# Performance work log

Hardware: AMD Instinct MI355X
Metric: run time of the kernel (lower is better)

## Reference

```python
import jax, jax.numpy as jnp
import numpy as np

B, S, D, H, F, E, TOPK, W = 1, 4096, 768, 12, 3072, 7, 2, 256  # W = one-sided window


def _layer_norm(x, g, b, eps=1e-5):
    m = jnp.mean(x, -1, keepdims=True)
    v = jnp.var(x, -1, keepdims=True)
    return (x - m) * jax.lax.rsqrt(v + eps) * g + b


def _sliding_attn(x, Wq, bq, Wk, bk, Wv, bv):
    # Longformer sliding-window attention, chunked (no dense SxS matrix).
    Bx, Sx, Dx = x.shape
    Dh = Dx // H
    def proj(Wm, bm):
        return (x @ Wm + bm).reshape(Bx, Sx, H, Dh).transpose(0, 2, 1, 3)  # [B,H,S,Dh]
    q = proj(Wq, bq) * (1.0 / np.sqrt(Dh))
    k = proj(Wk, bk)
    v = proj(Wv, bv)
    nc = Sx // W
    kp = jnp.pad(k, ((0, 0), (0, 0), (W, W), (0, 0)))
    vp = jnp.pad(v, ((0, 0), (0, 0), (W, W), (0, 0)))
    # each query chunk of W tokens sees a 3W key window
    idx = (jnp.arange(nc) * W)[:, None] + jnp.arange(3 * W)[None, :]  # [nc,3W]
    kc = kp[:, :, idx]  # [B,H,nc,3W,Dh]
    vc = vp[:, :, idx]
    qc = q.reshape(Bx, H, nc, W, Dh)
    scores = jnp.einsum('bhcqd,bhckd->bhcqk', qc, kc)  # [B,H,nc,W,3W]
    qi = jnp.arange(W)[:, None]
    ki = jnp.arange(3 * W)[None, :]
    band = (ki >= qi) & (ki <= qi + 2 * W)  # |key_pos - query_pos| <= W
    pos = (jnp.arange(nc) * W)[:, None, None] + ki[None] - W  # global key pos
    valid = band[None] & (pos >= 0) & (pos < Sx)  # [nc,W,3W]
    scores = jnp.where(valid[None, None], scores, -1e9)
    probs = jax.nn.softmax(scores, axis=-1)
    out = jnp.einsum('bhcqk,bhckd->bhcqd', probs, vc)
    return out.reshape(Bx, H, Sx, Dh).transpose(0, 2, 1, 3).reshape(Bx, Sx, Dx)


def setup_inputs() -> dict:
    key = jax.random.key(0)
    ks = jax.random.split(key, 16)
    sc = 0.02
    rn = lambda k, shp: jax.random.normal(k, shp, jnp.float32) * sc
    return {
        'hidden_states': jax.random.normal(ks[0], (B, S, D), jnp.float32),
        'Wq': rn(ks[1], (D, D)), 'bq': jnp.zeros((D,), jnp.float32),
        'Wk': rn(ks[2], (D, D)), 'bk': jnp.zeros((D,), jnp.float32),
        'Wv': rn(ks[3], (D, D)), 'bv': jnp.zeros((D,), jnp.float32),
        'Wo': rn(ks[4], (D, D)), 'bo': jnp.zeros((D,), jnp.float32),
        'ln1_g': jnp.ones((D,), jnp.float32), 'ln1_b': jnp.zeros((D,), jnp.float32),
        'gate_W': rn(ks[5], (D, E)), 'gate_b': jnp.zeros((E,), jnp.float32),
        'W1e': rn(ks[6], (E, D, F)), 'b1e': jnp.zeros((E, F), jnp.float32),
        'W2e': rn(ks[7], (E, F, D)), 'b2e': jnp.zeros((E, D), jnp.float32),
        'Wd': rn(ks[8], (D, D)), 'bd': jnp.zeros((D,), jnp.float32),
        'ln2_g': jnp.ones((D,), jnp.float32), 'ln2_b': jnp.zeros((D,), jnp.float32),
    }


def reference(hidden_states, Wq, bq, Wk, bk, Wv, bv, Wo, bo, ln1_g, ln1_b,
              gate_W, gate_b, W1e, b1e, W2e, b2e, Wd, bd, ln2_g, ln2_b):
    # attention + SelfOutput (dense + residual + LN); dropout = identity (eval)
    attn = _sliding_attn(hidden_states, Wq, bq, Wk, bk, Wv, bv)
    attention_output = _layer_norm(attn @ Wo + bo + hidden_states, ln1_g, ln1_b)
    # MoE feed-forward: dense all-experts compute, top-k masked softmax gate
    gate_logits = attention_output @ gate_W + gate_b  # [B,S,E]
    topv, topi = jax.lax.top_k(gate_logits, TOPK)
    # softmax over (-inf scatter of topk) == softmax over topk values scattered back
    sw = jax.nn.softmax(topv, axis=-1)  # [B,S,k]
    gate_weights = jnp.einsum('bske,bsk->bse',
                              jax.nn.one_hot(topi, E, dtype=attention_output.dtype), sw)
    h = jax.nn.gelu(jnp.einsum('bsd,edf->bsef', attention_output, W1e) + b1e,
                    approximate=False)  # [B,S,E,F]
    eo = jnp.einsum('bsef,efd->bsed', h, W2e) + b2e  # [B,S,E,D]
    moe = jnp.einsum('bsed,bse->bsd', eo, gate_weights)
    ffn = moe @ Wd + bd
    layer_output = _layer_norm(ffn + attention_output, ln2_g, ln2_b)
    return layer_output, gate_weights
```

## Files before the change

### kernel.cpp

```cpp
#include <hip/hip_runtime.h>
#include <math.h>

#define S_LEN 4096
#define DMODEL 768
#define NHEADS 12
#define DH 64
#define FDIM 3072
#define NEXP 7
#define NPAIR (2*S_LEN)
#define MAXTILES 40

typedef _Float16 f16x8 __attribute__((ext_vector_type(8)));
typedef float f32x4 __attribute__((ext_vector_type(4)));

__device__ __forceinline__ unsigned short f2h(float f){
  union { _Float16 h; unsigned short u; } v; v.h = (_Float16)f; return v.u;
}
__device__ __forceinline__ float gelu_f(float x){
  return 0.5f * x * (1.0f + erff(x * 0.7071067811865475f));
}
__device__ __forceinline__ f32x4 mfma16(f16x8 a, f16x8 b, f32x4 c){
  return __builtin_amdgcn_mfma_f32_16x16x32_f16(a, b, c, 0, 0, 0);
}
__device__ __forceinline__ void glds16(const void* g, void* l){
  __builtin_amdgcn_global_load_lds((const __attribute__((address_space(1))) unsigned*)g,
                                   (__attribute__((address_space(3))) unsigned*)l, 16, 0, 0);
}
__device__ __forceinline__ int xcd_logical(int lin, int total){
  int q = total >> 3;
  return (lin & 7)*q + (lin >> 3);
}

__global__ __launch_bounds__(256) void split_kernel(const float* __restrict__ in,
    unsigned short* __restrict__ out, int n){
  int i = blockIdx.x*256 + threadIdx.x;
  if (i >= n) return;
  out[i] = f2h(in[i]);
}

__global__ __launch_bounds__(256) void transp_kernel(const float* __restrict__ in,
    unsigned short* __restrict__ out,
    int R, int C, long inStride, long outStride){
  const float* ip = in + (long)blockIdx.z * inStride;
  long ob = (long)blockIdx.z * outStride;
  __shared__ float tile[32][33];
  int c0 = blockIdx.x*32, r0 = blockIdx.y*32;
  int tx = threadIdx.x, ty = threadIdx.y;
  for (int i = ty; i < 32; i += 8)
    tile[i][tx] = ip[(long)(r0+i)*C + c0 + tx];
  __syncthreads();
  int t  = tx + ty*32;
  int sx = t & 15;
  int sc = t >> 4;
  #pragma unroll
  for (int j = 0; j < 2; j++){
    int cc = sc + j*16;
    float v0 = tile[sx*2][cc], v1 = tile[sx*2+1][cc];
    long oidx = ob + (long)(c0+cc)*R + r0 + sx*2;
    unsigned uh = (unsigned)f2h(v0) | ((unsigned)f2h(v1) << 16);
    *(unsigned*)(out + oidx) = uh;
  }
}

struct GemmP {
  const unsigned short* A;
  const unsigned short* B;
  int M, N, K;
  const float* bias;  const float* bias2; const float* bias3;
  const float* resid;
  float* outF;
  unsigned short* outBF;
  unsigned short *qh,*kh,*vth;
  const int* pair_token;
  const float* pair_w;
  const int* cnt;
  const int* offs;
  const int* tile_e;
  const int* tile_m;
  const int* ntiles;
};

template<int MODE>
__global__ __launch_bounds__(256, 2) void gemm_bt(GemmP p){
  const int tid  = threadIdx.x;
  const int lane = tid & 63;
  const int wave = tid >> 6;
  const int quad = lane >> 4;
  const int ln   = lane & 15;
  const int wr = wave >> 1, wc = wave & 1;
  const int lin = blockIdx.y * gridDim.x + blockIdx.x;
  const int logical = xcd_logical(lin, gridDim.x*gridDim.y);
  const int bn0 = (logical % gridDim.x) * 128;
  const int bm0 = (logical / gridDim.x) * 128;
  const int K = p.K;

  long aoff[2]; long boff[2]; int koff[2];
  #pragma unroll
  for (int j = 0; j < 2; j++){
    int c = tid + j*256;
    int row = c >> 2;
    koff[j] = (c & 3) * 8;
    aoff[j] = (long)(bm0 + row) * K;
    boff[j] = (long)(bn0 + row) * K;
  }

  __shared__ __align__(16) unsigned short As[2][128*32];
  __shared__ __align__(16) unsigned short Bs[2][128*32];

  auto stage = [&](int k0, int buf){
    #pragma unroll
    for (int j = 0; j < 2; j++){
      int c = tid + j*256;
      glds16(p.A + aoff[j] + k0 + koff[j], &As[buf][c*8]);
      glds16(p.B + boff[j] + k0 + koff[j], &Bs[buf][c*8]);
    }
  };

  f32x4 zero4 = {0.f, 0.f, 0.f, 0.f};
  f32x4 acc[4][4];
  #pragma unroll
  for (int i = 0; i < 4; i++)
    #pragma unroll
    for (int j = 0; j < 4; j++) acc[i][j] = zero4;

  stage(0, 0);
  __syncthreads();
  int cur = 0;

  for (int k0 = 0; k0 < K; k0 += 32){
    if (k0 + 32 < K) stage(k0 + 32, cur ^ 1);
    f16x8 af[4], bfr[4];
    #pragma unroll
    for (int mt = 0; mt < 4; mt++)
      af[mt] = *(const f16x8*)&As[cur][(wr*64 + mt*16 + ln)*32 + quad*8];
    #pragma unroll
    for (int nt = 0; nt < 4; nt++)
      bfr[nt] = *(const f16x8*)&Bs[cur][(wc*64 + nt*16 + ln)*32 + quad*8];
    __builtin_amdgcn_s_setprio(1);
    #pragma unroll
    for (int mt = 0; mt < 4; mt++)
      #pragma unroll
      for (int nt = 0; nt < 4; nt++)
        acc[mt][nt] = mfma16(af[mt], bfr[nt], acc[mt][nt]);
    __builtin_amdgcn_s_setprio(0);
    asm volatile("s_waitcnt vmcnt(0)" ::: "memory");
    __builtin_amdgcn_s_barrier();
    cur ^= 1;
  }

  #pragma unroll
  for (int mt = 0; mt < 4; mt++){
    #pragma unroll
    for (int nt = 0; nt < 4; nt++){
      #pragma unroll
      for (int r = 0; r < 4; r++){
        int gm = bm0 + wr*64 + mt*16 + quad*4 + r;
        int gn = bn0 + wc*64 + nt*16 + ln;
        float v = acc[mt][nt][r];
        if (MODE == 0){
          int which = gn >= 1536 ? 2 : (gn >= 768 ? 1 : 0);
          int nn = gn - which*768;
          int hh = nn >> 6, dh = nn & 63;
          if (which == 0){
            float q = (v + p.bias[nn]) * 0.125f;
            long o = ((long)hh*S_LEN + gm)*64 + dh;
            p.qh[o] = f2h(q);
          } else if (which == 1){
            float kv = v + p.bias2[nn];
            long o = ((long)hh*S_LEN + gm)*64 + dh;
            p.kh[o] = f2h(kv);
          } else {
            float vv = v + p.bias3[nn];
            long o = ((long)hh*64 + dh)*S_LEN + gm;
            p.vth[o] = f2h(vv);
          }
        } else if (MODE == 1 || MODE == 4){
          long i = (long)gm*DMODEL + gn;
          p.outF[i] = v + p.bias[gn] + p.resid[i];
        }
      }
    }
  }
}

template<int MODE>
__global__ __launch_bounds__(512, 4) void gemm_big(GemmP p){
  const int lin = blockIdx.y * gridDim.x + blockIdx.x;
  const int logical = xcd_logical(lin, gridDim.x*gridDim.y);
  const int bx = logical % gridDim.x;
  const int ty = logical / gridDim.x;
  if (ty >= *p.ntiles) return;
  const int e   = p.tile_e[ty];
  const int bm0 = p.tile_m[ty];

  const int tid  = threadIdx.x;
  const int lane = tid & 63;
  const int wave = tid >> 6;
  const int quad = lane >> 4;
  const int ln   = lane & 15;
  const int wr = wave >> 1, wc = wave & 1;
  const int bn0 = bx * 128;
  const int K = p.K;

  const int eoff = p.offs[e];
  const int Mloc = p.cnt[e];
  const unsigned short* Bp = p.B + (long)e * FDIM * DMODEL;

  long aoff[2]; int koffA[2];
  #pragma unroll
  for (int j = 0; j < 2; j++){
    int c = tid + j*512;
    int row = c >> 2;
    koffA[j] = (c & 3) * 8;
    int r = bm0 + row; if (r >= Mloc) r = Mloc - 1;
    aoff[j] = (MODE == 2) ? (long)p.pair_token[eoff + r] * K : (long)(eoff + r) * K;
  }
  long boff; int koffB;
  {
    int row = tid >> 2;
    koffB = (tid & 3) * 8;
    boff = (long)(bn0 + row) * K;
  }

  __shared__ __align__(16) unsigned short As[2][256*32];
  __shared__ __align__(16) unsigned short Bs[2][128*32];

  auto stage = [&](int k0, int buf){
    #pragma unroll
    for (int j = 0; j < 2; j++){
      int c = tid + j*512;
      glds16(p.A + aoff[j] + k0 + koffA[j], &As[buf][c*8]);
    }
    glds16(Bp + boff + k0 + koffB, &Bs[buf][tid*8]);
  };

  f32x4 zero4 = {0.f, 0.f, 0.f, 0.f};
  f32x4 acc[4][4];
  #pragma unroll
  for (int i = 0; i < 4; i++)
    #pragma unroll
    for (int j = 0; j < 4; j++) acc[i][j] = zero4;

  stage(0, 0);
  __syncthreads();
  int cur = 0;

  for (int k0 = 0; k0 < K; k0 += 32){
    if (k0 + 32 < K) stage(k0 + 32, cur ^ 1);
    f16x8 af[4], bfr[4];
    #pragma unroll
    for (int mt = 0; mt < 4; mt++)
      af[mt] = *(const f16x8*)&As[cur][(wr*64 + mt*16 + ln)*32 + quad*8];
    #pragma unroll
    for (int nt = 0; nt < 4; nt++)
      bfr[nt] = *(const f16x8*)&Bs[cur][(wc*64 + nt*16 + ln)*32 + quad*8];
    __builtin_amdgcn_s_setprio(1);
    #pragma unroll
    for (int mt = 0; mt < 4; mt++)
      #pragma unroll
      for (int nt = 0; nt < 4; nt++)
        acc[mt][nt] = mfma16(af[mt], bfr[nt], acc[mt][nt]);
    __builtin_amdgcn_s_setprio(0);
    asm volatile("s_waitcnt vmcnt(0)" ::: "memory");
    __builtin_amdgcn_s_barrier();
    cur ^= 1;
  }

  #pragma unroll
  for (int mt = 0; mt < 4; mt++){
    #pragma unroll
    for (int nt = 0; nt < 4; nt++){
      #pragma unroll
      for (int r = 0; r < 4; r++){
        int gm = bm0 + wr*64 + mt*16 + quad*4 + r;
        int gn = bn0 + wc*64 + nt*16 + ln;
        if (gm < Mloc){
          float v = acc[mt][nt][r];
          if (MODE == 2){
            v = gelu_f(v + p.bias[(long)e*FDIM + gn]);
            p.outBF[(long)(eoff + gm)*FDIM + gn] = f2h(v);
          } else {
            int pi = eoff + gm;
            p.outF[(long)pi*DMODEL + gn] = v + p.bias[(long)e*DMODEL + gn];
          }
        }
      }
    }
  }
}

__global__ __launch_bounds__(256) void attn_mfma(
    const unsigned short* __restrict__ Qh,
    const unsigned short* __restrict__ Kh,
    const unsigned short* __restrict__ Vth,
    unsigned short* __restrict__ attn_h){
  const int c = blockIdx.x, h = blockIdx.y, qb = blockIdx.z;
  const int tid = threadIdx.x;
  const int lane = tid & 63, w = tid >> 6;
  const int quad = lane >> 4, ln = lane & 15;
  const int q0 = c*256 + qb*64;
  const int qw = q0 + w*16;

  __shared__ __align__(16) unsigned short Ks[64*64];
  __shared__ __align__(16) unsigned short Vs[64*64];
  __shared__ __align__(16) unsigned short Ps[4][16*72];

  f16x8 qf[2];
  {
    long qrow = ((long)h*S_LEN + qw + ln)*64 + quad*8;
    qf[0] = *(const f16x8*)(Qh + qrow);
    qf[1] = *(const f16x8*)(Qh + qrow + 32);
  }

  float m_s[4], l_s[4];
  f32x4 Oc[4];
  f32x4 z4 = {0.f,0.f,0.f,0.f};
  #pragma unroll
  for (int r = 0; r < 4; r++){ m_s[r] = -1e30f; l_s[r] = 0.f; }
  #pragma unroll
  for (int nt = 0; nt < 4; nt++) Oc[nt] = z4;

  const unsigned short* KB = Kh + (long)h*S_LEN*64;
  const unsigned short* VB = Vth + (long)h*64*S_LEN;

  for (int kb = 0; kb < 12; kb++){
    const int kstart = c*256 - 256 + kb*64;
    if (kstart + 63 < 0 || kstart >= S_LEN) continue;
    if (kstart + 63 < q0 - 256 || kstart > q0 + 63 + 256) continue;
    __syncthreads();
    #pragma unroll
    for (int p2 = 0; p2 < 2; p2++){
      int idx = p2*256 + tid;
      int row = idx >> 3;
      int pc  = idx & 7;
      int lc  = pc ^ (row & 7);
      int ka = kstart + row;
      int kac = ka < 0 ? 0 : (ka > S_LEN-1 ? S_LEN-1 : ka);
      long gK = (long)kac*64 + lc*8;
      glds16(KB + gK, &Ks[idx*8]);
      int ks0 = kstart + lc*8;
      ks0 = ks0 < 0 ? 0 : (ks0 > S_LEN-8 ? S_LEN-8 : ks0);
      long gV = (long)row*S_LEN + ks0;
      glds16(VB + gV, &Vs[idx*8]);
    }
    __syncthreads();
    if (kstart + 63 < qw - 256 || kstart > qw + 15 + 256) continue;

    f32x4 Sc[4];
    #pragma unroll
    for (int nt = 0; nt < 4; nt++) Sc[nt] = z4;
    #pragma unroll
    for (int kc = 0; kc < 2; kc++){
      f16x8 bh[4];
      #pragma unroll
      for (int nt = 0; nt < 4; nt++){
        int row = nt*16 + ln;
        int o = row*64 + (((kc*4 + quad) ^ (row & 7))*8);
        bh[nt] = *(const f16x8*)&Ks[o];
      }
      #pragma unroll
      for (int nt = 0; nt < 4; nt++)
        Sc[nt] = mfma16(qf[kc], bh[nt], Sc[nt]);
    }
    bool interior = (kstart >= qw - 241) && (kstart <= qw + 193) &&
                    (kstart >= 0) && (kstart + 63 <= S_LEN - 1);
    if (!interior){
      #pragma unroll
      for (int nt = 0; nt < 4; nt++){
        int ka = kstart + nt*16 + ln;
        #pragma unroll
        for (int r = 0; r < 4; r++){
          int qa = qw + quad*4 + r;
          bool v = (ka >= 0) && (ka < S_LEN) && (ka >= qa - 256) && (ka <= qa + 256);
          if (!v) Sc[nt][r] = -3.0e38f;
        }
      }
    }
    float bm[4];
    #pragma unroll
    for (int r = 0; r < 4; r++)
      bm[r] = fmaxf(fmaxf(Sc[0][r], Sc[1][r]), fmaxf(Sc[2][r], Sc[3][r]));
    #pragma unroll
    for (int off = 1; off < 16; off <<= 1)
      #pragma unroll
      for (int r = 0; r < 4; r++) bm[r] = fmaxf(bm[r], __shfl_xor(bm[r], off));
    float al[4];
    #pragma unroll
    for (int r = 0; r < 4; r++){
      float mnew = fmaxf(m_s[r], bm[r]);
      al[r] = __expf(m_s[r] - mnew);
      m_s[r] = mnew;
    }
    float psum[4] = {0.f,0.f,0.f,0.f};
    #pragma unroll
    for (int nt = 0; nt < 4; nt++){
      #pragma unroll
      for (int r = 0; r < 4; r++){
        float pv = __expf(Sc[nt][r] - m_s[r]);
        psum[r] += pv;
        int o = (quad*4 + r)*72 + nt*16 + ln;
        Ps[w][o] = f2h(pv);
      }
    }
    #pragma unroll
    for (int off = 1; off < 16; off <<= 1)
      #pragma unroll
      for (int r = 0; r < 4; r++) psum[r] += __shfl_xor(psum[r], off);
    #pragma unroll
    for (int r = 0; r < 4; r++) l_s[r] = l_s[r]*al[r] + psum[r];
    #pragma unroll
    for (int nt = 0; nt < 4; nt++)
      #pragma unroll
      for (int r = 0; r < 4; r++) Oc[nt][r] *= al[r];
    asm volatile("s_waitcnt lgkmcnt(0)" ::: "memory");
    #pragma unroll
    for (int kc = 0; kc < 2; kc++){
      f16x8 ph = *(const f16x8*)&Ps[w][ln*72 + kc*32 + quad*8];
      #pragma unroll
      for (int nt = 0; nt < 4; nt++){
        int row = nt*16 + ln;
        int o = row*64 + (((kc*4 + quad) ^ (row & 7))*8);
        f16x8 vh = *(const f16x8*)&Vs[o];
        Oc[nt] = mfma16(ph, vh, Oc[nt]);
      }
    }
  }
  float inv[4];
  #pragma unroll
  for (int r = 0; r < 4; r++) inv[r] = 1.f / l_s[r];
  #pragma unroll
  for (int nt = 0; nt < 4; nt++){
    #pragma unroll
    for (int r = 0; r < 4; r++){
      int qa = qw + quad*4 + r;
      long o = (long)qa*DMODEL + h*64 + nt*16 + ln;
      attn_h[o] = f2h(Oc[nt][r] * inv[r]);
    }
  }
}

__global__ __launch_bounds__(256) void ln_kernel(const float* __restrict__ x,
    const float* __restrict__ g, const float* __restrict__ b,
    float* __restrict__ outF, unsigned short* __restrict__ outH){
  int s = blockIdx.x;
  const float* row = x + (long)s*DMODEL;
  int t = threadIdx.x;
  float v0 = row[t], v1 = row[t+256], v2 = row[t+512];
  float sum = v0+v1+v2;
  float sq  = v0*v0 + v1*v1 + v2*v2;
  for (int o = 32; o > 0; o >>= 1){ sum += __shfl_xor(sum, o); sq += __shfl_xor(sq, o); }
  __shared__ float s1[4], s2[4];
  int wv = t >> 6;
  if ((t & 63) == 0){ s1[wv] = sum; s2[wv] = sq; }
  __syncthreads();
  sum = s1[0]+s1[1]+s1[2]+s1[3];
  sq  = s2[0]+s2[1]+s2[2]+s2[3];
  float mean = sum * (1.0f/DMODEL);
  float var  = sq  * (1.0f/DMODEL) - mean*mean;
  float inv = rsqrtf(var + 1e-5f);
  float* orow = outF + (long)s*DMODEL;
  unsigned short* hrow = outH ? outH + (long)s*DMODEL : (unsigned short*)0;
  #pragma unroll
  for (int j = 0; j < 3; j++){
    int d = t + j*256;
    float y = (row[d] - mean) * inv * g[d] + b[d];
    orow[d] = y;
    if (hrow) hrow[d] = f2h(y);
  }
}

__global__ __launch_bounds__(256) void gate_kernel(const float* __restrict__ x,
    const float* __restrict__ gw, const float* __restrict__ gb,
    float* __restrict__ gate_out, int* __restrict__ tok_e,
    float* __restrict__ tok_w){
  int w = threadIdx.x >> 6;
  int lane = threadIdx.x & 63;
  int s = blockIdx.x*4 + w;
  float acc[NEXP];
  #pragma unroll
  for (int e = 0; e < NEXP; e++) acc[e] = 0.f;
  const float* xr = x + (long)s*DMODEL;
  #pragma unroll
  for (int j = 0; j < DMODEL/64; j++){
    int d = lane + j*64;
    float xv = xr[d];
    const float* wr = gw + (long)d*NEXP;
    #pragma unroll
    for (int e = 0; e < NEXP; e++) acc[e] += xv * wr[e];
  }
  #pragma unroll
  for (int e = 0; e < NEXP; e++){
    float v = acc[e];
    for (int o = 32; o > 0; o >>= 1) v += __shfl_xor(v, o);
    acc[e] = v;
  }
  if (lane == 0){
    #pragma unroll
    for (int e = 0; e < NEXP; e++) acc[e] += gb[e];
    int i0 = 0;
    for (int e = 1; e < NEXP; e++) if (acc[e] > acc[i0]) i0 = e;
    int i1 = -1;
    for (int e = 0; e < NEXP; e++) if (e != i0 && (i1 < 0 || acc[e] > acc[i1])) i1 = e;
    float e1 = expf(acc[i1] - acc[i0]);
    float inv = 1.f / (1.f + e1);
    float w0 = inv, w1 = e1 * inv;
    float* go = gate_out + (long)s*NEXP;
    #pragma unroll
    for (int e = 0; e < NEXP; e++) go[e] = 0.f;
    go[i0] = w0; go[i1] = w1;
    tok_e[s*2] = i0; tok_e[s*2+1] = i1;
    tok_w[s*2] = w0; tok_w[s*2+1] = w1;
  }
}

__global__ __launch_bounds__(256) void route_kernel(const int* __restrict__ tok_e,
    const float* __restrict__ tok_w,
    int* __restrict__ cnt, int* __restrict__ offs,
    int* __restrict__ pair_token, float* __restrict__ pair_w, int* __restrict__ tok_pi,
    int* __restrict__ tile_e, int* __restrict__ tile_m, int* __restrict__ ntiles){
  __shared__ int hist[256][NEXP];
  __shared__ int cntS[NEXP], offsS[NEXP];
  const int t = threadIdx.x;
  const int CH = NPAIR/256;
  const int base = t*CH;
  #pragma unroll
  for (int e = 0; e < NEXP; e++) hist[t][e] = 0;
  for (int i = 0; i < CH; i++)
    hist[t][tok_e[base+i]]++;
  __syncthreads();
  if (t < NEXP){
    int s = 0;
    for (int i = 0; i < 256; i++){ int v = hist[i][t]; hist[i][t] = s; s += v; }
    cntS[t] = s;
  }
  __syncthreads();
  if (t == 0){
    int s = 0, tt = 0;
    for (int e = 0; e < NEXP; e++){ offsS[e] = s; s += cntS[e]; }
    for (int e = 0; e < NEXP; e++)
      for (int m0 = 0; m0 < cntS[e]; m0 += 256){ tile_e[tt] = e; tile_m[tt] = m0; tt++; }
    *ntiles = tt;
    for (int e = 0; e < NEXP; e++){ cnt[e] = cntS[e]; offs[e] = offsS[e]; }
  }
  __syncthreads();
  for (int i = 0; i < CH; i++){
    int idx = base + i;
    int e = tok_e[idx];
    int pi = offsS[e] + hist[t][e]++;
    pair_token[pi] = idx >> 1;
    pair_w[pi] = tok_w[idx];
    tok_pi[idx] = pi;
  }
}

__global__ __launch_bounds__(256) void combine_kernel(const float* __restrict__ Pbuf,
    const int* __restrict__ tok_pi, const float* __restrict__ tok_w,
    unsigned short* __restrict__ moe_h){
  int t = blockIdx.x;
  int d = threadIdx.x;
  float w0 = tok_w[t*2], w1 = tok_w[t*2+1];
  long p0 = (long)tok_pi[t*2]   * DMODEL;
  long p1 = (long)tok_pi[t*2+1] * DMODEL;
  unsigned short* orow = moe_h + (long)t*DMODEL;
  #pragma unroll
  for (int j = 0; j < 3; j++){
    int dd = d + j*256;
    orow[dd] = f2h(w0*Pbuf[p0+dd] + w1*Pbuf[p1+dd]);
  }
}

extern "C" void kernel_launch(void* const* d_in, const int* in_sizes, int n_in,
                              void* d_out, int out_size, void* d_ws, size_t ws_size,
                              hipStream_t stream){
  (void)in_sizes; (void)n_in; (void)out_size; (void)ws_size;
  const float* hidden = (const float*)d_in[0];
  const float* Wq  = (const float*)d_in[1];
  const float* bq  = (const float*)d_in[2];
  const float* Wk  = (const float*)d_in[3];
  const float* bk  = (const float*)d_in[4];
  const float* Wv  = (const float*)d_in[5];
  const float* bv  = (const float*)d_in[6];
  const float* Wo  = (const float*)d_in[7];
  const float* bo  = (const float*)d_in[8];
  const float* ln1g = (const float*)d_in[9];
  const float* ln1b = (const float*)d_in[10];
  const float* gateW = (const float*)d_in[11];
  const float* gateB = (const float*)d_in[12];
  const float* W1e = (const float*)d_in[13];
  const float* b1e = (const float*)d_in[14];
  const float* W2e = (const float*)d_in[15];
  const float* b2e = (const float*)d_in[16];
  const float* Wd  = (const float*)d_in[17];
  const float* bd  = (const float*)d_in[18];
  const float* ln2g = (const float*)d_in[19];
  const float* ln2b = (const float*)d_in[20];

  float* outL = (float*)d_out;
  float* outG = outL + (size_t)S_LEN*DMODEL;

  const size_t SD = (size_t)S_LEN*DMODEL;
  char* base = (char*)d_ws;
  size_t off = 0;
  auto alloc = [&](size_t bytes)->void*{
    void* r = base + off;
    off = (off + bytes + 255) & ~(size_t)255;
    return r;
  };
  unsigned short* x_h     = (unsigned short*)alloc(SD*2);
  unsigned short* wqkv_h  = (unsigned short*)alloc((size_t)2304*768*2);
  unsigned short* wo_h    = (unsigned short*)alloc((size_t)768*768*2);
  unsigned short* wd_h    = (unsigned short*)alloc((size_t)768*768*2);
  unsigned short* w1_h    = (unsigned short*)alloc((size_t)NEXP*FDIM*DMODEL*2);
  unsigned short* w2_h    = (unsigned short*)alloc((size_t)NEXP*FDIM*DMODEL*2);
  unsigned short* q_h   = (unsigned short*)alloc(SD*2);
  unsigned short* k_h   = (unsigned short*)alloc(SD*2);
  unsigned short* vt_h  = (unsigned short*)alloc(SD*2);
  unsigned short* attn_h = (unsigned short*)alloc(SD*2);
  float* preLN1    = (float*)alloc(SD*4);
  float* attnout_f = (float*)alloc(SD*4);
  unsigned short* attnout_h = (unsigned short*)alloc(SD*2);
  int*   tok_e = (int*)alloc(2*S_LEN*4);
  float* tok_w = (float*)alloc(2*S_LEN*4);
  int*   tok_pi = (int*)alloc(2*S_LEN*4);
  int*   cnt   = (int*)alloc(32*4);
  int*   offs  = (int*)alloc(32*4);
  int*   tile_e = (int*)alloc(MAXTILES*4);
  int*   tile_m = (int*)alloc(MAXTILES*4);
  int*   ntiles = (int*)alloc(4);
  int*   pair_token = (int*)alloc(NPAIR*4);
  float* pair_w     = (float*)alloc(NPAIR*4);
  unsigned short* Hbuf = (unsigned short*)alloc((size_t)NPAIR*FDIM*2);
  float* Pbuf = (float*)alloc((size_t)NPAIR*DMODEL*4);
  unsigned short* moe_h = (unsigned short*)alloc(SD*2);
  float* preLN2 = preLN1;

  split_kernel<<<dim3((unsigned)(SD/256)), dim3(256), 0, stream>>>(hidden, x_h, (int)SD);
  transp_kernel<<<dim3(24,24,1), dim3(32,8), 0, stream>>>(Wq, wqkv_h,           DMODEL, DMODEL, 0, 0);
  transp_kernel<<<dim3(24,24,1), dim3(32,8), 0, stream>>>(Wk, wqkv_h+768*768,   DMODEL, DMODEL, 0, 0);
  transp_kernel<<<dim3(24,24,1), dim3(32,8), 0, stream>>>(Wv, wqkv_h+2*768*768, DMODEL, DMODEL, 0, 0);
  transp_kernel<<<dim3(24,24,1), dim3(32,8), 0, stream>>>(Wo, wo_h, DMODEL, DMODEL, 0, 0);
  transp_kernel<<<dim3(24,24,1), dim3(32,8), 0, stream>>>(Wd, wd_h, DMODEL, DMODEL, 0, 0);
  transp_kernel<<<dim3(96,24,NEXP), dim3(32,8), 0, stream>>>(W1e, w1_h, DMODEL, FDIM, (long)DMODEL*FDIM, (long)DMODEL*FDIM);
  transp_kernel<<<dim3(24,96,NEXP), dim3(32,8), 0, stream>>>(W2e, w2_h, FDIM, DMODEL, (long)DMODEL*FDIM, (long)DMODEL*FDIM);

  GemmP pq = {};
  pq.A = x_h; pq.B = wqkv_h;
  pq.M = S_LEN; pq.N = 2304; pq.K = DMODEL;
  pq.bias = bq; pq.bias2 = bk; pq.bias3 = bv;
  pq.qh = q_h; pq.kh = k_h; pq.vth = vt_h;
  gemm_bt<0><<<dim3(18,32,1), dim3(256), 0, stream>>>(pq);

  attn_mfma<<<dim3(16,NHEADS,4), dim3(256), 0, stream>>>(q_h, k_h, vt_h, attn_h);

  GemmP pw = {};
  pw.A = attn_h; pw.B = wo_h;
  pw.M = S_LEN; pw.N = DMODEL; pw.K = DMODEL;
  pw.bias = bo; pw.resid = hidden; pw.outF = preLN1;
  gemm_bt<1><<<dim3(6,32,1), dim3(256), 0, stream>>>(pw);

  ln_kernel<<<dim3(S_LEN), dim3(256), 0, stream>>>(preLN1, ln1g, ln1b, attnout_f, attnout_h);

  gate_kernel<<<dim3(S_LEN/4), dim3(256), 0, stream>>>(attnout_f, gateW, gateB, outG, tok_e, tok_w);
  route_kernel<<<dim3(1), dim3(256), 0, stream>>>(tok_e, tok_w, cnt, offs,
      pair_token, pair_w, tok_pi, tile_e, tile_m, ntiles);

  GemmP p1 = {};
  p1.A = attnout_h; p1.B = w1_h; p1.M = S_LEN; p1.N = FDIM; p1.K = DMODEL;
  p1.bias = b1e; p1.outBF = Hbuf;
  p1.pair_token = pair_token; p1.cnt = cnt; p1.offs = offs;
  p1.tile_e = tile_e; p1.tile_m = tile_m; p1.ntiles = ntiles;
  gemm_big<2><<<dim3(24,MAXTILES), dim3(512), 0, stream>>>(p1);

  GemmP p2 = {};
  p2.A = Hbuf; p2.B = w2_h; p2.M = S_LEN; p2.N = DMODEL; p2.K = FDIM;
  p2.bias = b2e; p2.outF = Pbuf;
  p2.pair_token = pair_token; p2.pair_w = pair_w; p2.cnt = cnt; p2.offs = offs;
  p2.tile_e = tile_e; p2.tile_m = tile_m; p2.ntiles = ntiles;
  gemm_big<3><<<dim3(6,MAXTILES), dim3(512), 0, stream>>>(p2);

  combine_kernel<<<dim3(S_LEN), dim3(256), 0, stream>>>(Pbuf, tok_pi, tok_w, moe_h);
  GemmP pd = {};
  pd.A = moe_h; pd.B = wd_h; pd.M = S_LEN; pd.N = DMODEL; pd.K = DMODEL;
  pd.bias = bd; pd.resid = attnout_f; pd.outF = preLN2;
  gemm_bt<4><<<dim3(6,32,1), dim3(256), 0, stream>>>(pd);

  ln_kernel<<<dim3(S_LEN), dim3(256), 0, stream>>>(preLN2, ln2g, ln2b, outL, nullptr);
}
```

Before: 601.5 us.

## Swizzle GEMM LDS tiles, batch weight transposes, interleave MoE tile schedule

XOR-swizzles the 16-byte chunk position within each 32-element LDS row in both GEMM kernels, so the MFMA fragment reads spread across LDS banks instead of conflicting. Merges the five 768x768 weight transposes into one launch using a pointer table indexed by blockIdx.z. Reorders the MoE tile list into a strided interleave with -1 sentinels for empty slots, so consecutive blocks work on different experts and empty tiles exit early. The swizzle has to match between the global-to-LDS write and the fragment read, and the scatter into 8 groups of 5 slots assumes there are at most 40 tiles.

```diff
diff --git a/kernel.cpp b/kernel.cpp
--- a/kernel.cpp
+++ b/kernel.cpp
@@ -57,6 +57,29 @@
     int cc = sc + j*16;
     float v0 = tile[sx*2][cc], v1 = tile[sx*2+1][cc];
     long oidx = ob + (long)(c0+cc)*R + r0 + sx*2;
+    unsigned uh = (unsigned)f2h(v0) | ((unsigned)f2h(v1) << 16);
+    *(unsigned*)(out + oidx) = uh;
+  }
+}
+
+struct T5P { const float* in[5]; unsigned short* out[5]; };
+__global__ __launch_bounds__(256) void transp5_kernel(T5P p){
+  const float* ip = p.in[blockIdx.z];
+  unsigned short* out = p.out[blockIdx.z];
+  __shared__ float tile[32][33];
+  int c0 = blockIdx.x*32, r0 = blockIdx.y*32;
+  int tx = threadIdx.x, ty = threadIdx.y;
+  for (int i = ty; i < 32; i += 8)
+    tile[i][tx] = ip[(long)(r0+i)*DMODEL + c0 + tx];
+  __syncthreads();
+  int t  = tx + ty*32;
+  int sx = t & 15;
+  int sc = t >> 4;
+  #pragma unroll
+  for (int j = 0; j < 2; j++){
+    int cc = sc + j*16;
+    float v0 = tile[sx*2][cc], v1 = tile[sx*2+1][cc];
+    long oidx = (long)(c0+cc)*DMODEL + r0 + sx*2;
     unsigned uh = (unsigned)f2h(v0) | ((unsigned)f2h(v1) << 16);
     *(unsigned*)(out + oidx) = uh;
   }
@@ -99,7 +122,8 @@
   for (int j = 0; j < 2; j++){
     int c = tid + j*256;
     int row = c >> 2;
-    koff[j] = (c & 3) * 8;
+    int pc  = c & 3;
+    koff[j] = (pc ^ ((row >> 1) & 3)) * 8;
     aoff[j] = (long)(bm0 + row) * K;
     boff[j] = (long)(bn0 + row) * K;
   }
@@ -127,15 +151,17 @@
   __syncthreads();
   int cur = 0;
 
+  const int rsw = (quad ^ ((ln >> 1) & 3)) * 8;
+
   for (int k0 = 0; k0 < K; k0 += 32){
     if (k0 + 32 < K) stage(k0 + 32, cur ^ 1);
     f16x8 af[4], bfr[4];
     #pragma unroll
     for (int mt = 0; mt < 4; mt++)
-      af[mt] = *(const f16x8*)&As[cur][(wr*64 + mt*16 + ln)*32 + quad*8];
+      af[mt] = *(const f16x8*)&As[cur][(wr*64 + mt*16 + ln)*32 + rsw];
     #pragma unroll
     for (int nt = 0; nt < 4; nt++)
-      bfr[nt] = *(const f16x8*)&Bs[cur][(wc*64 + nt*16 + ln)*32 + quad*8];
+      bfr[nt] = *(const f16x8*)&Bs[cur][(wc*64 + nt*16 + ln)*32 + rsw];
     __builtin_amdgcn_s_setprio(1);
     #pragma unroll
     for (int mt = 0; mt < 4; mt++)
@@ -189,8 +215,8 @@
   const int logical = xcd_logical(lin, gridDim.x*gridDim.y);
   const int bx = logical % gridDim.x;
   const int ty = logical / gridDim.x;
-  if (ty >= *p.ntiles) return;
   const int e   = p.tile_e[ty];
+  if (e < 0) return;
   const int bm0 = p.tile_m[ty];
 
   const int tid  = threadIdx.x;
@@ -211,14 +237,16 @@
   for (int j = 0; j < 2; j++){
     int c = tid + j*512;
     int row = c >> 2;
-    koffA[j] = (c & 3) * 8;
+    int pc  = c & 3;
+    koffA[j] = (pc ^ ((row >> 1) & 3)) * 8;
     int r = bm0 + row; if (r >= Mloc) r = Mloc - 1;
     aoff[j] = (MODE == 2) ? (long)p.pair_token[eoff + r] * K : (long)(eoff + r) * K;
   }
   long boff; int koffB;
   {
     int row = tid >> 2;
-    koffB = (tid & 3) * 8;
+    int pc  = tid & 3;
+    koffB = (pc ^ ((row >> 1) & 3)) * 8;
     boff = (long)(bn0 + row) * K;
   }
 
@@ -245,15 +273,17 @@
   __syncthreads();
   int cur = 0;
 
+  const int rsw = (quad ^ ((ln >> 1) & 3)) * 8;
+
   for (int k0 = 0; k0 < K; k0 += 32){
     if (k0 + 32 < K) stage(k0 + 32, cur ^ 1);
     f16x8 af[4], bfr[4];
     #pragma unroll
     for (int mt = 0; mt < 4; mt++)
-      af[mt] = *(const f16x8*)&As[cur][(wr*64 + mt*16 + ln)*32 + quad*8];
+      af[mt] = *(const f16x8*)&As[cur][(wr*64 + mt*16 + ln)*32 + rsw];
     #pragma unroll
     for (int nt = 0; nt < 4; nt++)
-      bfr[nt] = *(const f16x8*)&Bs[cur][(wc*64 + nt*16 + ln)*32 + quad*8];
+      bfr[nt] = *(const f16x8*)&Bs[cur][(wc*64 + nt*16 + ln)*32 + rsw];
     __builtin_amdgcn_s_setprio(1);
     #pragma unroll
     for (int mt = 0; mt < 4; mt++)
@@ -536,9 +566,15 @@
   __syncthreads();
   if (t == 0){
     int s = 0, tt = 0;
+    int te[MAXTILES], tm[MAXTILES];
     for (int e = 0; e < NEXP; e++){ offsS[e] = s; s += cntS[e]; }
     for (int e = 0; e < NEXP; e++)
-      for (int m0 = 0; m0 < cntS[e]; m0 += 256){ tile_e[tt] = e; tile_m[tt] = m0; tt++; }
+      for (int m0 = 0; m0 < cntS[e]; m0 += 256){ te[tt] = e; tm[tt] = m0; tt++; }
+    for (int p2 = 0; p2 < MAXTILES; p2++){ tile_e[p2] = -1; tile_m[p2] = 0; }
+    for (int t2 = 0; t2 < tt; t2++){
+      int pos = (t2 & 7)*(MAXTILES/8) + (t2 >> 3);
+      tile_e[pos] = te[t2]; tile_m[pos] = tm[t2];
+    }
     *ntiles = tt;
     for (int e = 0; e < NEXP; e++){ cnt[e] = cntS[e]; offs[e] = offsS[e]; }
   }
@@ -635,11 +671,13 @@
   float* preLN2 = preLN1;
 
   split_kernel<<<dim3((unsigned)(SD/256)), dim3(256), 0, stream>>>(hidden, x_h, (int)SD);
-  transp_kernel<<<dim3(24,24,1), dim3(32,8), 0, stream>>>(Wq, wqkv_h,           DMODEL, DMODEL, 0, 0);
-  transp_kernel<<<dim3(24,24,1), dim3(32,8), 0, stream>>>(Wk, wqkv_h+768*768,   DMODEL, DMODEL, 0, 0);
-  transp_kernel<<<dim3(24,24,1), dim3(32,8), 0, stream>>>(Wv, wqkv_h+2*768*768, DMODEL, DMODEL, 0, 0);
-  transp_kernel<<<dim3(24,24,1), dim3(32,8), 0, stream>>>(Wo, wo_h, DMODEL, DMODEL, 0, 0);
-  transp_kernel<<<dim3(24,24,1), dim3(32,8), 0, stream>>>(Wd, wd_h, DMODEL, DMODEL, 0, 0);
+  T5P t5;
+  t5.in[0] = Wq; t5.out[0] = wqkv_h;
+  t5.in[1] = Wk; t5.out[1] = wqkv_h + 768*768;
+  t5.in[2] = Wv; t5.out[2] = wqkv_h + 2*768*768;
+  t5.in[3] = Wo; t5.out[3] = wo_h;
+  t5.in[4] = Wd; t5.out[4] = wd_h;
+  transp5_kernel<<<dim3(24,24,5), dim3(32,8), 0, stream>>>(t5);
   transp_kernel<<<dim3(96,24,NEXP), dim3(32,8), 0, stream>>>(W1e, w1_h, DMODEL, FDIM, (long)DMODEL*FDIM, (long)DMODEL*FDIM);
   transp_kernel<<<dim3(24,96,NEXP), dim3(32,8), 0, stream>>>(W2e, w2_h, FDIM, DMODEL, (long)DMODEL*FDIM, (long)DMODEL*FDIM);
 
```

Result: no change. 610.5 us (+1.5%).
